# Performance work log

Hardware: AMD Instinct MI355X
Metric: run time of the kernel (lower is better)

The kernel has to match this reference:

```python
import jax, jax.numpy as jnp
import numpy as np

DEP_NUM, HEAD_NUM, BSZ, DIM, REL = 96, 96, 16, 512, 128


def setup_inputs() -> dict:
    key = jax.random.key(0)
    k1, k2, k3, k4 = jax.random.split(key, 4)
    outs = jax.random.normal(k1, (DEP_NUM, BSZ, DIM), dtype=jnp.float32)
    graph_state = jax.random.normal(k2, (HEAD_NUM, BSZ, DIM), dtype=jnp.float32)
    # nn.init.normal_(std=0.02) for both weights, zero biases
    Wt = 0.02 * jax.random.normal(k3, (DIM, 2 * DIM), dtype=jnp.float32)
    bt = jnp.zeros((DIM,), dtype=jnp.float32)
    Wp = 0.02 * jax.random.normal(k4, (REL, DIM), dtype=jnp.float32)
    bp = jnp.zeros((REL,), dtype=jnp.float32)
    return {"outs": outs, "graph_state": graph_state, "Wt": Wt, "bt": bt, "Wp": Wp, "bp": bp}


def reference(outs, graph_state, Wt, bt, Wp, bp):
    # outs: [dep, b, D], graph_state: [head, b, D]
    # Linear(cat(dep, head)) == dep @ Wt[:, :D].T + head @ Wt[:, D:].T + bt
    D = outs.shape[-1]
    dep_proj = jnp.einsum('dbi,ei->dbe', outs, Wt[:, :D])           # [dep, b, D]
    head_proj = jnp.einsum('hbi,ei->hbe', graph_state, Wt[:, D:])   # [head, b, D]
    # broadcast-sum to pairwise: [dep, b, head, D]
    h = jax.nn.relu(dep_proj[:, :, None, :] + jnp.swapaxes(head_proj, 0, 1)[None] + bt)
    # dropout: identity in eval mode
    scores = jnp.einsum('dbhe,re->dbhr', h, Wp) + bp                # [dep, b, head, REL]
    nil = jnp.zeros(scores.shape[:-1] + (1,), dtype=scores.dtype)
    scores = jnp.concatenate([nil, scores], axis=-1)                # [dep, b, head, REL+1]
    return jax.nn.log_softmax(scores, axis=-1)
```

## Files before the change

kernel.cpp:

```cpp
#include <hip/hip_runtime.h>
#include <hip/hip_bf16.h>
#include <math.h>

#define DEP   96
#define HEADS 96
#define BSZ   16
#define DIM   512
#define REL   128
#define RELP  129

typedef __attribute__((ext_vector_type(8))) short short8;
typedef __attribute__((ext_vector_type(4))) float floatx4;

__device__ __forceinline__ unsigned short f2bf(float x) {
    union { float f; unsigned int u; } c; c.f = x;
    unsigned int r = c.u + 0x7fffu + ((c.u >> 16) & 1u);
    return (unsigned short)(r >> 16);
}
__device__ __forceinline__ float bflo2f(unsigned int u) {
    union { unsigned int u; float f; } c; c.u = u << 16; return c.f;
}
__device__ __forceinline__ float bfhi2f(unsigned int u) {
    union { unsigned int u; float f; } c; c.u = u & 0xffff0000u; return c.f;
}

#define PSS 72

__global__ __launch_bounds__(256) void proj_kernel(
    const float* __restrict__ outs, const float* __restrict__ graph,
    const float* __restrict__ Wt,   const float* __restrict__ bt,
    float* __restrict__ P1, unsigned short* __restrict__ P2B)
{
    const int z = blockIdx.z;
    const float* A = z ? graph : outs;
    const int off  = z ? DIM : 0;
    const int row0 = blockIdx.y * 64;
    const int col0 = blockIdx.x * 64;

    __shared__ unsigned short As[64 * PSS];
    __shared__ unsigned short Ws[64 * PSS];

    const int tid  = threadIdx.x;
    const int lane = tid & 63;
    const int wv   = tid >> 6;
    const int ln15 = lane & 15;
    const int quad = lane >> 4;

    floatx4 acc[4];
    #pragma unroll
    for (int nt = 0; nt < 4; ++nt) acc[nt] = (floatx4){0.f,0.f,0.f,0.f};

    for (int kt = 0; kt < DIM; kt += 64) {
        #pragma unroll
        for (int q = 0; q < 4; ++q) {
            const int slot = q*256 + tid;
            const int r  = slot >> 4;
            const int e4 = (slot & 15) * 4;
            float4 v = *(const float4*)(A + (size_t)(row0 + r) * DIM + kt + e4);
            ushort4 o;
            o.x = f2bf(v.x); o.y = f2bf(v.y); o.z = f2bf(v.z); o.w = f2bf(v.w);
            *(ushort4*)&As[r * PSS + e4] = o;
        }
        #pragma unroll
        for (int q = 0; q < 4; ++q) {
            const int slot = q*256 + tid;
            const int r  = slot >> 4;
            const int e4 = (slot & 15) * 4;
            float4 v = *(const float4*)(Wt + (size_t)(col0 + r) * (2*DIM) + off + kt + e4);
            ushort4 o;
            o.x = f2bf(v.x); o.y = f2bf(v.y); o.z = f2bf(v.z); o.w = f2bf(v.w);
            *(ushort4*)&Ws[r * PSS + e4] = o;
        }
        __syncthreads();
        #pragma unroll
        for (int ks = 0; ks < 64; ks += 32) {
            short8 af = *(const short8*)&As[(wv*16 + ln15) * PSS + ks + quad*8];
            #pragma unroll
            for (int nt = 0; nt < 4; ++nt) {
                short8 bf8 = *(const short8*)&Ws[(nt*16 + ln15) * PSS + ks + quad*8];
                acc[nt] = __builtin_amdgcn_mfma_f32_16x16x32_bf16(af, bf8, acc[nt], 0, 0, 0);
            }
        }
        __syncthreads();
    }

    #pragma unroll
    for (int nt = 0; nt < 4; ++nt) {
        #pragma unroll
        for (int reg = 0; reg < 4; ++reg) {
            const int m = row0 + wv*16 + quad*4 + reg;
            const int n = col0 + nt*16 + ln15;
            float v = acc[nt][reg];
            if (!z) P1[(size_t)m * DIM + n] = v + bt[n];
            else    P2B[(size_t)m * DIM + n] = f2bf(v);
        }
    }
}

__global__ __launch_bounds__(256) void wp_cvt_kernel(
    const float* __restrict__ Wp, unsigned short* __restrict__ WpB)
{
    const int i = blockIdx.x * 256 + threadIdx.x;
    float4 v = *(const float4*)(Wp + (size_t)i * 4);
    ushort4 o;
    o.x = f2bf(v.x); o.y = f2bf(v.y); o.z = f2bf(v.z); o.w = f2bf(v.w);
    *(ushort4*)(WpB + (size_t)i * 4) = o;
}

#define HSS 72
#define WSS 72

__global__ __launch_bounds__(128, 2) void fused_kernel(
    const float* __restrict__ P1, const unsigned short* __restrict__ P2B,
    const unsigned short* __restrict__ WpB, const float* __restrict__ bp,
    float* __restrict__ out)
{
    const int db = blockIdx.x;
    const int b  = db & 15;

    __shared__ float          drow[DIM];
    __shared__ unsigned short hs[96 * HSS];
    __shared__ unsigned short ws[128 * WSS];

    const int tid  = threadIdx.x;
    const int lane = tid & 63;
    const int wv   = tid >> 6;
    const int ln15 = lane & 15;
    const int quad = lane >> 4;

    #pragma unroll
    for (int q = 0; q < 4; ++q) drow[q*128 + tid] = P1[(size_t)db * DIM + q*128 + tid];
    __syncthreads();

    floatx4 acc[3][8];
    #pragma unroll
    for (int i = 0; i < 3; ++i)
        #pragma unroll
        for (int j = 0; j < 8; ++j) acc[i][j] = (floatx4){0.f,0.f,0.f,0.f};

    for (int kt = 0; kt < DIM; kt += 64) {
        #pragma unroll
        for (int q = 0; q < 6; ++q) {
            const int slot = q*128 + tid;
            const int h  = slot >> 3;
            const int e8 = (slot & 7) * 8;
            uint4 pv = *(const uint4*)(P2B + ((size_t)h * BSZ + b) * DIM + kt + e8);
            float4 d0 = *(const float4*)&drow[kt + e8];
            float4 d1 = *(const float4*)&drow[kt + e8 + 4];
            float s0 = fmaxf(bflo2f(pv.x) + d0.x, 0.f);
            float s1 = fmaxf(bfhi2f(pv.x) + d0.y, 0.f);
            float s2 = fmaxf(bflo2f(pv.y) + d0.z, 0.f);
            float s3 = fmaxf(bfhi2f(pv.y) + d0.w, 0.f);
            float s4 = fmaxf(bflo2f(pv.z) + d1.x, 0.f);
            float s5 = fmaxf(bfhi2f(pv.z) + d1.y, 0.f);
            float s6 = fmaxf(bflo2f(pv.w) + d1.z, 0.f);
            float s7 = fmaxf(bfhi2f(pv.w) + d1.w, 0.f);
            uint2 o0, o1;
            o0.x = (unsigned)f2bf(s0) | ((unsigned)f2bf(s1) << 16);
            o0.y = (unsigned)f2bf(s2) | ((unsigned)f2bf(s3) << 16);
            o1.x = (unsigned)f2bf(s4) | ((unsigned)f2bf(s5) << 16);
            o1.y = (unsigned)f2bf(s6) | ((unsigned)f2bf(s7) << 16);
            *(uint2*)&hs[h * HSS + e8]     = o0;
            *(uint2*)&hs[h * HSS + e8 + 4] = o1;
        }
        #pragma unroll
        for (int q = 0; q < 8; ++q) {
            const int slot = q*128 + tid;
            const int r = slot >> 3;
            const int g = (slot & 7) * 8;
            uint4 v = *(const uint4*)(WpB + (size_t)r * DIM + kt + g);
            *(uint4*)&ws[r * WSS + g] = v;
        }
        __syncthreads();

        #pragma unroll
        for (int ks = 0; ks < 64; ks += 32) {
            short8 af[3], bf8[8];
            #pragma unroll
            for (int mt = 0; mt < 3; ++mt)
                af[mt] = *(const short8*)&hs[(wv*48 + mt*16 + ln15) * HSS + ks + quad*8];
            #pragma unroll
            for (int nt = 0; nt < 8; ++nt)
                bf8[nt] = *(const short8*)&ws[(nt*16 + ln15) * WSS + ks + quad*8];
            #pragma unroll
            for (int nt = 0; nt < 8; ++nt)
                #pragma unroll
                for (int mt = 0; mt < 3; ++mt)
                    acc[mt][nt] = __builtin_amdgcn_mfma_f32_16x16x32_bf16(
                        af[mt], bf8[nt], acc[mt][nt], 0, 0, 0);
        }
        __syncthreads();
    }

    float bpv[8];
    #pragma unroll
    for (int nt = 0; nt < 8; ++nt) bpv[nt] = bp[nt*16 + ln15];

    #pragma unroll
    for (int mt = 0; mt < 3; ++mt) {
        #pragma unroll
        for (int reg = 0; reg < 4; ++reg) {
            const int m = wv*48 + mt*16 + quad*4 + reg;
            float s[8];
            float mx = 0.f;
            #pragma unroll
            for (int nt = 0; nt < 8; ++nt) {
                s[nt] = acc[mt][nt][reg] + bpv[nt];
                mx = fmaxf(mx, s[nt]);
            }
            #pragma unroll
            for (int msk = 1; msk < 16; msk <<= 1) mx = fmaxf(mx, __shfl_xor(mx, msk));
            float l = 0.f;
            #pragma unroll
            for (int nt = 0; nt < 8; ++nt) l += __expf(s[nt] - mx);
            #pragma unroll
            for (int msk = 1; msk < 16; msk <<= 1) l += __shfl_xor(l, msk);
            l += __expf(-mx);
            const float lse = mx + __logf(l);

            const size_t base = ((size_t)db * HEADS + m) * RELP;
            #pragma unroll
            for (int nt = 0; nt < 8; ++nt) out[base + 1 + nt*16 + ln15] = s[nt] - lse;
            if (ln15 == 0) out[base] = -lse;
        }
    }
}

extern "C" void kernel_launch(void* const* d_in, const int* in_sizes, int n_in,
                              void* d_out, int out_size, void* d_ws, size_t ws_size,
                              hipStream_t stream) {
    const float* outs  = (const float*)d_in[0];
    const float* graph = (const float*)d_in[1];
    const float* Wt    = (const float*)d_in[2];
    const float* bt    = (const float*)d_in[3];
    const float* Wp    = (const float*)d_in[4];
    const float* bp    = (const float*)d_in[5];
    float* out = (float*)d_out;

    float* P1 = (float*)d_ws;
    unsigned short* P2B = (unsigned short*)(P1 + (size_t)DEP * BSZ * DIM);
    unsigned short* WpB = P2B + (size_t)DEP * BSZ * DIM;

    wp_cvt_kernel<<<REL * DIM / (256 * 4), 256, 0, stream>>>(Wp, WpB);
    proj_kernel<<<dim3(DIM/64, (DEP*BSZ)/64, 2), 256, 0, stream>>>(
        outs, graph, Wt, bt, P1, P2B);
    fused_kernel<<<DEP*BSZ, 128, 0, stream>>>(P1, P2B, WpB, bp, out);
}
```

Baseline: 163.9 us.

## Split fused kernel's REL dimension across 4 waves; pre-convert Wt to bf16

The fused kernel now uses 256 threads, with each wave covering 48 heads by 64 relation columns instead of 48 by 128. This halves the accumulator registers per thread and raises occupancy. The log-softmax is now combined across the two column halves through a small shared-memory exchange of per-row max and sum, which adds a barrier. Separately, Wt is converted to bf16 once in a merged conversion kernel, so the projection GEMM no longer converts the weight tile on every pass and loads half as many bytes.

Measured after the change: 161.0 us. About the same (-1.8%).

```diff
diff --git a/kernel.cpp b/kernel.cpp
--- a/kernel.cpp
+++ b/kernel.cpp
@@ -24,11 +24,29 @@
     union { unsigned int u; float f; } c; c.u = u & 0xffff0000u; return c.f;
 }
 
+__global__ __launch_bounds__(256) void cvt_kernel(
+    const float* __restrict__ Wt, const float* __restrict__ Wp,
+    unsigned short* __restrict__ WtB, unsigned short* __restrict__ WpB)
+{
+    const int chunk = blockIdx.x * 256 + threadIdx.x;
+    const float* src; unsigned short* dst; int c;
+    if (chunk < 65536) { src = Wt; dst = WtB; c = chunk; }
+    else               { src = Wp; dst = WpB; c = chunk - 65536; }
+    float4 a = *(const float4*)(src + (size_t)c * 8);
+    float4 b = *(const float4*)(src + (size_t)c * 8 + 4);
+    uint4 o;
+    o.x = (unsigned)f2bf(a.x) | ((unsigned)f2bf(a.y) << 16);
+    o.y = (unsigned)f2bf(a.z) | ((unsigned)f2bf(a.w) << 16);
+    o.z = (unsigned)f2bf(b.x) | ((unsigned)f2bf(b.y) << 16);
+    o.w = (unsigned)f2bf(b.z) | ((unsigned)f2bf(b.w) << 16);
+    *(uint4*)(dst + (size_t)c * 8) = o;
+}
+
 #define PSS 72
 
 __global__ __launch_bounds__(256) void proj_kernel(
     const float* __restrict__ outs, const float* __restrict__ graph,
-    const float* __restrict__ Wt,   const float* __restrict__ bt,
+    const unsigned short* __restrict__ WtB, const float* __restrict__ bt,
     float* __restrict__ P1, unsigned short* __restrict__ P2B)
 {
     const int z = blockIdx.z;
@@ -62,14 +80,12 @@
             *(ushort4*)&As[r * PSS + e4] = o;
         }
         #pragma unroll
-        for (int q = 0; q < 4; ++q) {
-            const int slot = q*256 + tid;
-            const int r  = slot >> 4;
-            const int e4 = (slot & 15) * 4;
-            float4 v = *(const float4*)(Wt + (size_t)(col0 + r) * (2*DIM) + off + kt + e4);
-            ushort4 o;
-            o.x = f2bf(v.x); o.y = f2bf(v.y); o.z = f2bf(v.z); o.w = f2bf(v.w);
-            *(ushort4*)&Ws[r * PSS + e4] = o;
+        for (int q = 0; q < 2; ++q) {
+            const int slot = q*256 + tid;
+            const int r  = slot >> 3;
+            const int e8 = (slot & 7) * 8;
+            *(uint4*)&Ws[r * PSS + e8] =
+                *(const uint4*)(WtB + (size_t)(col0 + r) * (2*DIM) + off + kt + e8);
         }
         __syncthreads();
         #pragma unroll
@@ -97,20 +113,10 @@
     }
 }
 
-__global__ __launch_bounds__(256) void wp_cvt_kernel(
-    const float* __restrict__ Wp, unsigned short* __restrict__ WpB)
-{
-    const int i = blockIdx.x * 256 + threadIdx.x;
-    float4 v = *(const float4*)(Wp + (size_t)i * 4);
-    ushort4 o;
-    o.x = f2bf(v.x); o.y = f2bf(v.y); o.z = f2bf(v.z); o.w = f2bf(v.w);
-    *(ushort4*)(WpB + (size_t)i * 4) = o;
-}
-
 #define HSS 72
 #define WSS 72
 
-__global__ __launch_bounds__(128, 2) void fused_kernel(
+__global__ __launch_bounds__(256, 4) void fused_kernel(
     const float* __restrict__ P1, const unsigned short* __restrict__ P2B,
     const unsigned short* __restrict__ WpB, const float* __restrict__ bp,
     float* __restrict__ out)
@@ -121,27 +127,31 @@
     __shared__ float          drow[DIM];
     __shared__ unsigned short hs[96 * HSS];
     __shared__ unsigned short ws[128 * WSS];
+    __shared__ float          pmx[96][2];
+    __shared__ float          pl [96][2];
 
     const int tid  = threadIdx.x;
     const int lane = tid & 63;
     const int wv   = tid >> 6;
     const int ln15 = lane & 15;
     const int quad = lane >> 4;
-
-    #pragma unroll
-    for (int q = 0; q < 4; ++q) drow[q*128 + tid] = P1[(size_t)db * DIM + q*128 + tid];
+    const int mh   = wv & 1;
+    const int nh   = wv >> 1;
+
+    drow[tid]       = P1[(size_t)db * DIM + tid];
+    drow[tid + 256] = P1[(size_t)db * DIM + tid + 256];
     __syncthreads();
 
-    floatx4 acc[3][8];
+    floatx4 acc[3][4];
     #pragma unroll
     for (int i = 0; i < 3; ++i)
         #pragma unroll
-        for (int j = 0; j < 8; ++j) acc[i][j] = (floatx4){0.f,0.f,0.f,0.f};
+        for (int j = 0; j < 4; ++j) acc[i][j] = (floatx4){0.f,0.f,0.f,0.f};
 
     for (int kt = 0; kt < DIM; kt += 64) {
         #pragma unroll
-        for (int q = 0; q < 6; ++q) {
-            const int slot = q*128 + tid;
+        for (int q = 0; q < 3; ++q) {
+            const int slot = q*256 + tid;
             const int h  = slot >> 3;
             const int e8 = (slot & 7) * 8;
             uint4 pv = *(const uint4*)(P2B + ((size_t)h * BSZ + b) * DIM + kt + e8);
@@ -155,35 +165,34 @@
             float s5 = fmaxf(bfhi2f(pv.z) + d1.y, 0.f);
             float s6 = fmaxf(bflo2f(pv.w) + d1.z, 0.f);
             float s7 = fmaxf(bfhi2f(pv.w) + d1.w, 0.f);
-            uint2 o0, o1;
-            o0.x = (unsigned)f2bf(s0) | ((unsigned)f2bf(s1) << 16);
-            o0.y = (unsigned)f2bf(s2) | ((unsigned)f2bf(s3) << 16);
-            o1.x = (unsigned)f2bf(s4) | ((unsigned)f2bf(s5) << 16);
-            o1.y = (unsigned)f2bf(s6) | ((unsigned)f2bf(s7) << 16);
-            *(uint2*)&hs[h * HSS + e8]     = o0;
-            *(uint2*)&hs[h * HSS + e8 + 4] = o1;
-        }
-        #pragma unroll
-        for (int q = 0; q < 8; ++q) {
-            const int slot = q*128 + tid;
+            uint4 o;
+            o.x = (unsigned)f2bf(s0) | ((unsigned)f2bf(s1) << 16);
+            o.y = (unsigned)f2bf(s2) | ((unsigned)f2bf(s3) << 16);
+            o.z = (unsigned)f2bf(s4) | ((unsigned)f2bf(s5) << 16);
+            o.w = (unsigned)f2bf(s6) | ((unsigned)f2bf(s7) << 16);
+            *(uint4*)&hs[h * HSS + e8] = o;
+        }
+        #pragma unroll
+        for (int q = 0; q < 4; ++q) {
+            const int slot = q*256 + tid;
             const int r = slot >> 3;
             const int g = (slot & 7) * 8;
-            uint4 v = *(const uint4*)(WpB + (size_t)r * DIM + kt + g);
-            *(uint4*)&ws[r * WSS + g] = v;
+            *(uint4*)&ws[r * WSS + g] =
+                *(const uint4*)(WpB + (size_t)r * DIM + kt + g);
         }
         __syncthreads();
 
         #pragma unroll
         for (int ks = 0; ks < 64; ks += 32) {
-            short8 af[3], bf8[8];
+            short8 af[3], bf8[4];
             #pragma unroll
             for (int mt = 0; mt < 3; ++mt)
-                af[mt] = *(const short8*)&hs[(wv*48 + mt*16 + ln15) * HSS + ks + quad*8];
-            #pragma unroll
-            for (int nt = 0; nt < 8; ++nt)
-                bf8[nt] = *(const short8*)&ws[(nt*16 + ln15) * WSS + ks + quad*8];
-            #pragma unroll
-            for (int nt = 0; nt < 8; ++nt)
+                af[mt] = *(const short8*)&hs[(mh*48 + mt*16 + ln15) * HSS + ks + quad*8];
+            #pragma unroll
+            for (int nt = 0; nt < 4; ++nt)
+                bf8[nt] = *(const short8*)&ws[(nh*64 + nt*16 + ln15) * WSS + ks + quad*8];
+            #pragma unroll
+            for (int nt = 0; nt < 4; ++nt)
                 #pragma unroll
                 for (int mt = 0; mt < 3; ++mt)
                     acc[mt][nt] = __builtin_amdgcn_mfma_f32_16x16x32_bf16(
@@ -192,19 +201,19 @@
         __syncthreads();
     }
 
-    float bpv[8];
-    #pragma unroll
-    for (int nt = 0; nt < 8; ++nt) bpv[nt] = bp[nt*16 + ln15];
+    float bpv[4];
+    #pragma unroll
+    for (int nt = 0; nt < 4; ++nt) bpv[nt] = bp[nh*64 + nt*16 + ln15];
 
     #pragma unroll
     for (int mt = 0; mt < 3; ++mt) {
         #pragma unroll
         for (int reg = 0; reg < 4; ++reg) {
-            const int m = wv*48 + mt*16 + quad*4 + reg;
-            float s[8];
-            float mx = 0.f;
-            #pragma unroll
-            for (int nt = 0; nt < 8; ++nt) {
+            const int m = mh*48 + mt*16 + quad*4 + reg;
+            float s[4];
+            float mx = -1e30f;
+            #pragma unroll
+            for (int nt = 0; nt < 4; ++nt) {
                 s[nt] = acc[mt][nt][reg] + bpv[nt];
                 mx = fmaxf(mx, s[nt]);
             }
@@ -212,16 +221,31 @@
             for (int msk = 1; msk < 16; msk <<= 1) mx = fmaxf(mx, __shfl_xor(mx, msk));
             float l = 0.f;
             #pragma unroll
-            for (int nt = 0; nt < 8; ++nt) l += __expf(s[nt] - mx);
+            for (int nt = 0; nt < 4; ++nt) l += __expf(s[nt] - mx);
             #pragma unroll
             for (int msk = 1; msk < 16; msk <<= 1) l += __shfl_xor(l, msk);
-            l += __expf(-mx);
-            const float lse = mx + __logf(l);
+            if (ln15 == 0) { pmx[m][nh] = mx; pl[m][nh] = l; }
+        }
+    }
+    __syncthreads();
+
+    #pragma unroll
+    for (int mt = 0; mt < 3; ++mt) {
+        #pragma unroll
+        for (int reg = 0; reg < 4; ++reg) {
+            const int m = mh*48 + mt*16 + quad*4 + reg;
+            const float mx0 = pmx[m][0], mx1 = pmx[m][1];
+            const float l0  = pl[m][0],  l1  = pl[m][1];
+            const float MX = fmaxf(fmaxf(mx0, mx1), 0.f);
+            const float L  = l0 * __expf(mx0 - MX) + l1 * __expf(mx1 - MX)
+                           + __expf(-MX);
+            const float lse = MX + __logf(L);
 
             const size_t base = ((size_t)db * HEADS + m) * RELP;
             #pragma unroll
-            for (int nt = 0; nt < 8; ++nt) out[base + 1 + nt*16 + ln15] = s[nt] - lse;
-            if (ln15 == 0) out[base] = -lse;
+            for (int nt = 0; nt < 4; ++nt)
+                out[base + 1 + nh*64 + nt*16 + ln15] = acc[mt][nt][reg] + bpv[nt] - lse;
+            if (nh == 0 && ln15 == 0) out[base] = -lse;
         }
     }
 }
@@ -237,12 +261,13 @@
     const float* bp    = (const float*)d_in[5];
     float* out = (float*)d_out;
 
-    float* P1 = (float*)d_ws;
-    unsigned short* P2B = (unsigned short*)(P1 + (size_t)DEP * BSZ * DIM);
-    unsigned short* WpB = P2B + (size_t)DEP * BSZ * DIM;
-
-    wp_cvt_kernel<<<REL * DIM / (256 * 4), 256, 0, stream>>>(Wp, WpB);
+    float* P1           = (float*)d_ws;
+    unsigned short* P2B = (unsigned short*)(P1 + 786432);
+    unsigned short* WpB = P2B + 786432;
+    unsigned short* WtB = WpB + 65536;
+
+    cvt_kernel<<<288, 256, 0, stream>>>(Wt, Wp, WtB, WpB);
     proj_kernel<<<dim3(DIM/64, (DEP*BSZ)/64, 2), 256, 0, stream>>>(
-        outs, graph, Wt, bt, P1, P2B);
-    fused_kernel<<<DEP*BSZ, 128, 0, stream>>>(P1, P2B, WpB, bp, out);
-}
+        outs, graph, WtB, bt, P1, P2B);
+    fused_kernel<<<DEP*BSZ, 256, 0, stream>>>(P1, P2B, WpB, bp, out);
+}
```
